# Kernel tuning notes

Measured on AMD Instinct MI355X. Metric: run time of the kernel, lower is better.

The kernel has to match this reference:

```python
import jax, jax.numpy as jnp
import numpy as np

N, K, A = 4096, 64, 8      # nodes, level-2 paths per node, attrs per l2-neighbor
D = 128                    # embed_dim
NU, NR, NA = 100000, 32, 5000  # user vocab, rating vocab, attribute vocab


def setup_inputs() -> dict:
    key = jax.random.key(0)
    ks = jax.random.split(key, 12)
    s = 0.02
    return dict(
        nodes=jax.random.randint(ks[0], (N,), 0, NU),
        paths_rel=jax.random.randint(ks[1], (N, K, 2), 0, NR),
        paths_nbr=jax.random.randint(ks[2], (N, K), 0, NU),
        attrs=jax.random.randint(ks[3], (N, K, A), 0, NA),
        u2e=jax.random.normal(ks[4], (NU, D), dtype=jnp.float32) * s,
        r2e=jax.random.normal(ks[5], (NR, D), dtype=jnp.float32) * s,
        ua2e=jax.random.normal(ks[6], (NA, D), dtype=jnp.float32) * s,
        W1=jax.random.normal(ks[7], (4 * D, 2 * D), dtype=jnp.float32) * s,
        b1=jnp.zeros((2 * D,), jnp.float32),
        W2=jax.random.normal(ks[8], (2 * D, D), dtype=jnp.float32) * s,
        b2=jnp.zeros((D,), jnp.float32),
        A1=jax.random.normal(ks[9], (2 * D, D), dtype=jnp.float32) * s,
        ab1=jnp.zeros((D,), jnp.float32),
        A2=jax.random.normal(ks[10], (D, D), dtype=jnp.float32) * s,
        ab2=jnp.zeros((D,), jnp.float32),
        A3=jax.random.normal(ks[11], (D, 1), dtype=jnp.float32) * s,
        ab3=jnp.zeros((1,), jnp.float32),
    )


def reference(nodes, paths_rel, paths_nbr, attrs, u2e, r2e, ua2e,
              W1, b1, W2, b2, A1, ab1, A2, ab2, A3, ab3):
    # per-path embedding gathers
    r1 = r2e[paths_rel[..., 0]]           # [N,K,D]
    r2 = r2e[paths_rel[..., 1]]           # [N,K,D]
    ne = u2e[paths_nbr]                   # [N,K,D]
    ae = ua2e[attrs].sum(axis=2)          # [N,K,A,D] -> [N,K,D] (uvAttrEmbedding sum)
    # concat + 2-layer MLP (w_r1, w_r2)
    x = jnp.concatenate([r1, r2, ne, ae], axis=-1)   # [N,K,4D]
    h = jax.nn.relu(x @ W1 + b1)                     # [N,K,2D]
    h = jax.nn.relu(h @ W2 + b2)                     # [N,K,D]
    # attention vs self embedding
    self_e = u2e[nodes]                              # [N,D]
    c = jnp.concatenate(
        [h, jnp.broadcast_to(self_e[:, None, :], h.shape)], axis=-1)  # [N,K,2D]
    a = jax.nn.relu(c @ A1 + ab1)
    a = jax.nn.relu(a @ A2 + ab2)
    logits = (a @ A3 + ab3)[..., 0]                  # [N,K]
    w = jax.nn.softmax(logits, axis=1)
    # attention-weighted reduce over paths
    return jnp.einsum('nk,nkd->nd', w, h)            # [N,D]
```

## Files before the change

### kernel.cpp

```cpp
#include <hip/hip_runtime.h>
#include <hip/hip_bf16.h>

#define NN 4096
#define KK 64
#define AA 8
#define DD 128

#define XH_STRIDE 264
#define A_STRIDE  136
#define H2_STRIDE 136
#define XREG_SZ   16896

typedef __bf16 bf16x8 __attribute__((ext_vector_type(8)));
typedef __bf16 bf16x2 __attribute__((ext_vector_type(2)));
typedef float  f32x4  __attribute__((ext_vector_type(4)));

__device__ __forceinline__ short f2bf(float f) {
    unsigned u = __builtin_bit_cast(unsigned, f);
    u += 0x7FFFu + ((u >> 16) & 1u);
    return (short)(u >> 16);
}
__device__ __forceinline__ float bf2f(short s) {
    unsigned u = ((unsigned)(unsigned short)s) << 16;
    return __builtin_bit_cast(float, u);
}
__device__ __forceinline__ unsigned f2bf2(float a, float b) {
#if __has_builtin(__builtin_amdgcn_cvt_pk_bf16_f32)
    bf16x2 r = __builtin_amdgcn_cvt_pk_bf16_f32(a, b);
    return __builtin_bit_cast(unsigned, r);
#else
    return ((unsigned)(unsigned short)f2bf(a)) | (((unsigned)(unsigned short)f2bf(b)) << 16);
#endif
}
__device__ __forceinline__ void store_bf8(short* dst, float4 a, float4 b) {
    uint4 v;
    v.x = f2bf2(a.x, a.y); v.y = f2bf2(a.z, a.w);
    v.z = f2bf2(b.x, b.y); v.w = f2bf2(b.z, b.w);
    *(uint4*)dst = v;
}
__device__ __forceinline__ void store_bf4(short* dst, float4 a) {
    uint2 v;
    v.x = f2bf2(a.x, a.y); v.y = f2bf2(a.z, a.w);
    *(uint2*)dst = v;
}

__global__ void prep_all(const float* __restrict__ W1, const float* __restrict__ W2,
                         const float* __restrict__ A1, const float* __restrict__ A2,
                         const int* __restrict__ nodes, const float* __restrict__ u2e,
                         const float* __restrict__ ab1,
                         short* __restrict__ W1p, short* __restrict__ W2p,
                         short* __restrict__ A1p, short* __restrict__ A2p,
                         float* __restrict__ s1g)
{
    if (blockIdx.x < 768) {
        int t = blockIdx.x * 256 + threadIdx.x;
        const float* src; short* dst; int Ncols, ksl, idx;
        if (t < 131072)      { src = W1; dst = W1p; Ncols = 256; ksl = 4; idx = t; }
        else if (t < 163840) { src = W2; dst = W2p; Ncols = 128; ksl = 3; idx = t - 131072; }
        else if (t < 180224) { src = A1; dst = A1p; Ncols = 128; ksl = 2; idx = t - 163840; }
        else                 { src = A2; dst = A2p; Ncols = 128; ksl = 2; idx = t - 180224; }
        int j     = idx & 7;
        int lane  = (idx >> 3) & 63;
        int fi    = idx >> 9;
        int kstep = fi & ((1 << ksl) - 1);
        int ntile = fi >> ksl;
        int k  = kstep * 32 + (lane >> 4) * 8 + j;
        int nn = ntile * 16 + (lane & 15);
        dst[idx] = f2bf(src[(size_t)k * Ncols + nn]);
    } else {
        __shared__ float rows[8][DD];
        const int b = blockIdx.x - 768;
        {
            const int r  = threadIdx.x >> 5;
            const int c4 = (threadIdx.x & 31) * 4;
            const int node = nodes[b * 8 + r];
            *(float4*)&rows[r][c4] = *(const float4*)&u2e[(size_t)node * DD + c4];
        }
        __syncthreads();
        const int h = threadIdx.x >> 7;
        const int c = threadIdx.x & 127;
        const float ab = ab1[c];
        float acc[4] = {ab, ab, ab, ab};
        for (int i = 0; i < DD; ++i) {
            const float av = A1[(size_t)(DD + i) * DD + c];
#pragma unroll
            for (int j = 0; j < 4; ++j)
                acc[j] = fmaf(rows[h * 4 + j][i], av, acc[j]);
        }
#pragma unroll
        for (int j = 0; j < 4; ++j)
            s1g[(size_t)(b * 8 + h * 4 + j) * DD + c] = acc[j];
    }
}

__launch_bounds__(512, 4)
__global__ void l2agg_mfma(
    const int* __restrict__ paths_rel,
    const int* __restrict__ paths_nbr,
    const int* __restrict__ attrs,
    const float* __restrict__ u2e,
    const float* __restrict__ r2e,
    const float* __restrict__ ua2e,
    const float* __restrict__ b1,
    const float* __restrict__ b2,
    const float* __restrict__ ab2,
    const float* __restrict__ A3,
    const float* __restrict__ ab3,
    const short* __restrict__ W1p,
    const short* __restrict__ W2p,
    const short* __restrict__ A1p,
    const short* __restrict__ A2p,
    const float* __restrict__ s1g,
    float* __restrict__ out)
{
    __shared__ short xa[XREG_SZ];
    __shared__ short xb[XREG_SZ];
    __shared__ int idx_u[576];
    float* partials = (float*)idx_u;
    float* wts      = (float*)(idx_u + 512);

    const int n    = blockIdx.x;
    const int tid  = threadIdx.x;
    const int lane = tid & 63;
    const int wv   = tid >> 6;
    const int mr   = lane & 15;
    const int q    = lane >> 4;

    {
        const int* ab = attrs + (size_t)n * KK * AA;
        __builtin_amdgcn_global_load_lds(
            (const __attribute__((address_space(1))) void*)(ab + wv * 64 + lane),
            (__attribute__((address_space(3))) void*)(idx_u + wv * 64), 4, 0, 0);
        if (wv == 0) {
            const int* nb = paths_nbr + (size_t)n * KK;
            __builtin_amdgcn_global_load_lds(
                (const __attribute__((address_space(1))) void*)(nb + lane),
                (__attribute__((address_space(3))) void*)(idx_u + 512), 4, 0, 0);
        }
    }

#pragma unroll
    for (int pass = 0; pass < 2; ++pass) {
        const int p  = pass * 32 + (tid >> 4);
        const int t  = tid & 15;
        const int o  = t * 8;
        const int pk = n * KK + p;
        const int i0 = paths_rel[pk * 2 + 0];
        const int i1 = paths_rel[pk * 2 + 1];
        float4 r1a = *(const float4*)&r2e[(size_t)i0 * DD + o];
        float4 r1b = *(const float4*)&r2e[(size_t)i0 * DD + o + 4];
        float4 r2a = *(const float4*)&r2e[(size_t)i1 * DD + o];
        float4 r2b = *(const float4*)&r2e[(size_t)i1 * DD + o + 4];
        store_bf8(&xa[p * XH_STRIDE + o], r1a, r1b);
        store_bf8(&xa[p * XH_STRIDE + 128 + o], r2a, r2b);
    }
    __syncthreads();

    const short* W1b = W1p + wv * 2 * 16 * 512 + lane * 8;
    f32x4 acc1[4][2] = {};
    bf16x8 bfc[2], bfn[2];
#pragma unroll
    for (int nt = 0; nt < 2; ++nt) bfc[nt] = *(const bf16x8*)&W1b[nt * 8192];

    const int sp = tid >> 5;
    const int so = (tid & 31) * 4;

#pragma unroll
    for (int step = 0; step < 4; ++step) {
        const int p  = step * 16 + sp;
        const int nb = idx_u[512 + p];
        const int4 ai0 = *(const int4*)&idx_u[p * 8];
        const int4 ai1 = *(const int4*)&idx_u[p * 8 + 4];
        float4 nev = *(const float4*)&u2e[(size_t)nb * DD + so];
        float4 g0 = *(const float4*)&ua2e[(size_t)ai0.x * DD + so];
        float4 g1 = *(const float4*)&ua2e[(size_t)ai0.y * DD + so];
        float4 g2 = *(const float4*)&ua2e[(size_t)ai0.z * DD + so];
        float4 g3 = *(const float4*)&ua2e[(size_t)ai0.w * DD + so];
        {
            const int ks = 2 * step;
#pragma unroll
            for (int nt = 0; nt < 2; ++nt)
                bfn[nt] = *(const bf16x8*)&W1b[nt * 8192 + (ks + 1) * 512];
            bf16x8 af[4];
#pragma unroll
            for (int mt = 0; mt < 4; ++mt)
                af[mt] = *(const bf16x8*)&xa[(mt * 16 + mr) * XH_STRIDE + ks * 32 + q * 8];
#pragma unroll
            for (int nt = 0; nt < 2; ++nt)
#pragma unroll
                for (int mt = 0; mt < 4; ++mt)
                    acc1[mt][nt] = __builtin_amdgcn_mfma_f32_16x16x32_bf16(af[mt], bfc[nt], acc1[mt][nt], 0, 0, 0);
#pragma unroll
            for (int nt = 0; nt < 2; ++nt) bfc[nt] = bfn[nt];
        }
        float4 s4;
        s4.x = (g0.x + g1.x) + (g2.x + g3.x);
        s4.y = (g0.y + g1.y) + (g2.y + g3.y);
        s4.z = (g0.z + g1.z) + (g2.z + g3.z);
        s4.w = (g0.w + g1.w) + (g2.w + g3.w);
        store_bf4(&xb[p * XH_STRIDE + so], nev);
        float4 g4 = *(const float4*)&ua2e[(size_t)ai1.x * DD + so];
        float4 g5 = *(const float4*)&ua2e[(size_t)ai1.y * DD + so];
        float4 g6 = *(const float4*)&ua2e[(size_t)ai1.z * DD + so];
        float4 g7 = *(const float4*)&ua2e[(size_t)ai1.w * DD + so];
        {
            const int ks = 2 * step + 1;
#pragma unroll
            for (int nt = 0; nt < 2; ++nt)
                bfn[nt] = *(const bf16x8*)&W1b[nt * 8192 + (ks + 1) * 512];
            bf16x8 af[4];
#pragma unroll
            for (int mt = 0; mt < 4; ++mt)
                af[mt] = *(const bf16x8*)&xa[(mt * 16 + mr) * XH_STRIDE + ks * 32 + q * 8];
#pragma unroll
            for (int nt = 0; nt < 2; ++nt)
#pragma unroll
                for (int mt = 0; mt < 4; ++mt)
                    acc1[mt][nt] = __builtin_amdgcn_mfma_f32_16x16x32_bf16(af[mt], bfc[nt], acc1[mt][nt], 0, 0, 0);
#pragma unroll
            for (int nt = 0; nt < 2; ++nt) bfc[nt] = bfn[nt];
        }
        s4.x += (g4.x + g5.x) + (g6.x + g7.x);
        s4.y += (g4.y + g5.y) + (g6.y + g7.y);
        s4.z += (g4.z + g5.z) + (g6.z + g7.z);
        s4.w += (g4.w + g5.w) + (g6.w + g7.w);
        store_bf4(&xb[p * XH_STRIDE + 128 + so], s4);
    }
    __syncthreads();

#pragma unroll
    for (int ks = 8; ks < 16; ++ks) {
        if (ks < 15) {
#pragma unroll
            for (int nt = 0; nt < 2; ++nt)
                bfn[nt] = *(const bf16x8*)&W1b[nt * 8192 + (ks + 1) * 512];
        }
        bf16x8 af[4];
#pragma unroll
        for (int mt = 0; mt < 4; ++mt)
            af[mt] = *(const bf16x8*)&xb[(mt * 16 + mr) * XH_STRIDE + (ks - 8) * 32 + q * 8];
#pragma unroll
        for (int nt = 0; nt < 2; ++nt)
#pragma unroll
            for (int mt = 0; mt < 4; ++mt)
                acc1[mt][nt] = __builtin_amdgcn_mfma_f32_16x16x32_bf16(af[mt], bfc[nt], acc1[mt][nt], 0, 0, 0);
        if (ks < 15) {
#pragma unroll
            for (int nt = 0; nt < 2; ++nt) bfc[nt] = bfn[nt];
        }
    }

    const short* W2b = W2p + wv * 8 * 512 + lane * 8;
    bf16x8 g2c = *(const bf16x8*)&W2b[0], g2n;

#pragma unroll
    for (int nt = 0; nt < 2; ++nt) {
        const int col = (wv * 2 + nt) * 16 + mr;
        const float bb = b1[col];
#pragma unroll
        for (int mt = 0; mt < 4; ++mt)
#pragma unroll
            for (int r = 0; r < 4; r += 2) {
                unsigned pk2 = f2bf2(fmaxf(acc1[mt][nt][r] + bb, 0.f),
                                     fmaxf(acc1[mt][nt][r + 1] + bb, 0.f));
                xa[(mt * 16 + q * 4 + r)     * XH_STRIDE + col] = (short)pk2;
                xa[(mt * 16 + q * 4 + r + 1) * XH_STRIDE + col] = (short)(pk2 >> 16);
            }
    }
    __syncthreads();

    f32x4 acc2[4] = {};
#pragma unroll
    for (int ks = 0; ks < 8; ++ks) {
        if (ks < 7) g2n = *(const bf16x8*)&W2b[(ks + 1) * 512];
        bf16x8 af[4];
#pragma unroll
        for (int mt = 0; mt < 4; ++mt)
            af[mt] = *(const bf16x8*)&xa[(mt * 16 + mr) * XH_STRIDE + ks * 32 + q * 8];
#pragma unroll
        for (int mt = 0; mt < 4; ++mt)
            acc2[mt] = __builtin_amdgcn_mfma_f32_16x16x32_bf16(af[mt], g2c, acc2[mt], 0, 0, 0);
        if (ks < 7) g2c = g2n;
    }

    const short* A1b = A1p + wv * 4 * 512 + lane * 8;
    bf16x8 g3f[4];
#pragma unroll
    for (int ks = 0; ks < 4; ++ks) g3f[ks] = *(const bf16x8*)&A1b[ks * 512];
    const float s1v = s1g[(size_t)n * DD + wv * 16 + mr];

    {
        const int col = wv * 16 + mr;
        const float bb = b2[col];
#pragma unroll
        for (int mt = 0; mt < 4; ++mt)
#pragma unroll
            for (int r = 0; r < 4; r += 2) {
                unsigned pk2 = f2bf2(fmaxf(acc2[mt][r] + bb, 0.f),
                                     fmaxf(acc2[mt][r + 1] + bb, 0.f));
                xb[(mt * 16 + q * 4 + r)     * H2_STRIDE + col] = (short)pk2;
                xb[(mt * 16 + q * 4 + r + 1) * H2_STRIDE + col] = (short)(pk2 >> 16);
            }
    }
    __syncthreads();

    {
        f32x4 acc3[4];
#pragma unroll
        for (int mt = 0; mt < 4; ++mt) {
            acc3[mt][0] = s1v; acc3[mt][1] = s1v; acc3[mt][2] = s1v; acc3[mt][3] = s1v;
        }
#pragma unroll
        for (int ks = 0; ks < 4; ++ks) {
            bf16x8 af[4];
#pragma unroll
            for (int mt = 0; mt < 4; ++mt)
                af[mt] = *(const bf16x8*)&xb[(mt * 16 + mr) * H2_STRIDE + ks * 32 + q * 8];
#pragma unroll
            for (int mt = 0; mt < 4; ++mt)
                acc3[mt] = __builtin_amdgcn_mfma_f32_16x16x32_bf16(af[mt], g3f[ks], acc3[mt], 0, 0, 0);
        }
        const short* A2b = A2p + wv * 4 * 512 + lane * 8;
        bf16x8 g4f[4];
#pragma unroll
        for (int ks = 0; ks < 4; ++ks) g4f[ks] = *(const bf16x8*)&A2b[ks * 512];

        {
            const int col = wv * 16 + mr;
#pragma unroll
            for (int mt = 0; mt < 4; ++mt)
#pragma unroll
                for (int r = 0; r < 4; r += 2) {
                    unsigned pk2 = f2bf2(fmaxf(acc3[mt][r], 0.f),
                                         fmaxf(acc3[mt][r + 1], 0.f));
                    xa[(mt * 16 + q * 4 + r)     * A_STRIDE + col] = (short)pk2;
                    xa[(mt * 16 + q * 4 + r + 1) * A_STRIDE + col] = (short)(pk2 >> 16);
                }
        }
        __syncthreads();

        f32x4 acc4[4];
        {
            const float bv = ab2[wv * 16 + mr];
#pragma unroll
            for (int mt = 0; mt < 4; ++mt) {
                acc4[mt][0] = bv; acc4[mt][1] = bv; acc4[mt][2] = bv; acc4[mt][3] = bv;
            }
        }
#pragma unroll
        for (int ks = 0; ks < 4; ++ks) {
            bf16x8 af[4];
#pragma unroll
            for (int mt = 0; mt < 4; ++mt)
                af[mt] = *(const bf16x8*)&xa[(mt * 16 + mr) * A_STRIDE + ks * 32 + q * 8];
#pragma unroll
            for (int mt = 0; mt < 4; ++mt)
                acc4[mt] = __builtin_amdgcn_mfma_f32_16x16x32_bf16(af[mt], g4f[ks], acc4[mt], 0, 0, 0);
        }
        const float av = A3[wv * 16 + mr];
        float pl[4][4];
#pragma unroll
        for (int mt = 0; mt < 4; ++mt)
#pragma unroll
            for (int r = 0; r < 4; ++r)
                pl[mt][r] = fmaxf(acc4[mt][r], 0.f) * av;
#pragma unroll
        for (int off = 1; off < 16; off <<= 1)
#pragma unroll
            for (int mt = 0; mt < 4; ++mt)
#pragma unroll
                for (int r = 0; r < 4; ++r)
                    pl[mt][r] += __shfl_xor(pl[mt][r], off, 64);
        if (mr == 0) {
#pragma unroll
            for (int mt = 0; mt < 4; ++mt)
#pragma unroll
                for (int r = 0; r < 4; ++r)
                    partials[wv * KK + mt * 16 + q * 4 + r] = pl[mt][r];
        }
    }
    __syncthreads();

    if (tid < KK) {
        float l = ab3[0];
#pragma unroll
        for (int w = 0; w < 8; ++w) l += partials[w * KK + tid];
        float m = l;
#pragma unroll
        for (int off = 32; off > 0; off >>= 1) m = fmaxf(m, __shfl_xor(m, off, 64));
        float e = expf(l - m);
        float s = e;
#pragma unroll
        for (int off = 32; off > 0; off >>= 1) s += __shfl_xor(s, off, 64);
        wts[tid] = e / s;
    }
    __syncthreads();

    if (tid < DD) {
        float acc = 0.f;
#pragma unroll 8
        for (int k = 0; k < KK; ++k)
            acc = fmaf(wts[k], bf2f(xb[k * H2_STRIDE + tid]), acc);
        out[(size_t)n * DD + tid] = acc;
    }
}

extern "C" void kernel_launch(void* const* d_in, const int* in_sizes, int n_in,
                              void* d_out, int out_size, void* d_ws, size_t ws_size,
                              hipStream_t stream)
{
    const int*   nodes     = (const int*)d_in[0];
    const int*   paths_rel = (const int*)d_in[1];
    const int*   paths_nbr = (const int*)d_in[2];
    const int*   attrs     = (const int*)d_in[3];
    const float* u2e  = (const float*)d_in[4];
    const float* r2e  = (const float*)d_in[5];
    const float* ua2e = (const float*)d_in[6];
    const float* W1   = (const float*)d_in[7];
    const float* b1   = (const float*)d_in[8];
    const float* W2   = (const float*)d_in[9];
    const float* b2   = (const float*)d_in[10];
    const float* A1   = (const float*)d_in[11];
    const float* ab1  = (const float*)d_in[12];
    const float* A2   = (const float*)d_in[13];
    const float* ab2  = (const float*)d_in[14];
    const float* A3   = (const float*)d_in[15];
    const float* ab3  = (const float*)d_in[16];
    float* out = (float*)d_out;

    short* wsp = (short*)d_ws;
    short* W1p = wsp;
    short* W2p = wsp + 131072;
    short* A1p = wsp + 163840;
    short* A2p = wsp + 180224;
    float* s1g = (float*)((char*)d_ws + 393216);

    hipLaunchKernelGGL(prep_all, dim3(768 + 512), dim3(256), 0, stream,
                       W1, W2, A1, A2, nodes, u2e, ab1,
                       W1p, W2p, A1p, A2p, s1g);
    hipLaunchKernelGGL(l2agg_mfma, dim3(NN), dim3(512), 0, stream,
                       paths_rel, paths_nbr, attrs, u2e, r2e, ua2e,
                       b1, b2, ab2, A3, ab3,
                       W1p, W2p, A1p, A2p, s1g, out);
}
```

Before: 298.0 us.

## Reorder W1 first-half MFMA before gathers, retile W2 GEMM, parallelize final reduce

The first half of the W1 GEMM now runs as a tight MFMA loop, and the neighbor and attribute gathers happen afterwards, with each thread loading 8-wide vectors. This replaces the earlier interleaving of gathers with MFMA steps. The W2 GEMM is retiled so each wave computes a 2x2 block of 16x16 tiles instead of 4 M-tiles by 1 N-tile, which reuses A fragments across two B fragments. The softmax and weighted reduction now run redundantly in every wave: each wave recomputes the softmax over the 64 logits and reduces its own 16 columns with a shuffle reduction, which removes a barrier. The trade-off is that gather latency is no longer hidden behind matrix work, and the softmax is computed eight times.

```diff
diff --git a/kernel.cpp b/kernel.cpp
--- a/kernel.cpp
+++ b/kernel.cpp
@@ -37,11 +37,6 @@
     v.x = f2bf2(a.x, a.y); v.y = f2bf2(a.z, a.w);
     v.z = f2bf2(b.x, b.y); v.w = f2bf2(b.z, b.w);
     *(uint4*)dst = v;
-}
-__device__ __forceinline__ void store_bf4(short* dst, float4 a) {
-    uint2 v;
-    v.x = f2bf2(a.x, a.y); v.y = f2bf2(a.z, a.w);
-    *(uint2*)dst = v;
 }
 
 __global__ void prep_all(const float* __restrict__ W1, const float* __restrict__ W2,
@@ -115,9 +110,9 @@
 {
     __shared__ short xa[XREG_SZ];
     __shared__ short xb[XREG_SZ];
-    __shared__ int idx_u[576];
+    __shared__ int   idx_u[576];
+    __shared__ float wts8[512];
     float* partials = (float*)idx_u;
-    float* wts      = (float*)(idx_u + 512);
 
     const int n    = blockIdx.x;
     const int tid  = threadIdx.x;
@@ -161,79 +156,53 @@
     bf16x8 bfc[2], bfn[2];
 #pragma unroll
     for (int nt = 0; nt < 2; ++nt) bfc[nt] = *(const bf16x8*)&W1b[nt * 8192];
-
-    const int sp = tid >> 5;
-    const int so = (tid & 31) * 4;
-
-#pragma unroll
-    for (int step = 0; step < 4; ++step) {
-        const int p  = step * 16 + sp;
+#pragma unroll
+    for (int ks = 0; ks < 8; ++ks) {
+#pragma unroll
+        for (int nt = 0; nt < 2; ++nt)
+            bfn[nt] = *(const bf16x8*)&W1b[nt * 8192 + (ks + 1) * 512];
+        bf16x8 af[4];
+#pragma unroll
+        for (int mt = 0; mt < 4; ++mt)
+            af[mt] = *(const bf16x8*)&xa[(mt * 16 + mr) * XH_STRIDE + ks * 32 + q * 8];
+#pragma unroll
+        for (int nt = 0; nt < 2; ++nt)
+#pragma unroll
+            for (int mt = 0; mt < 4; ++mt)
+                acc1[mt][nt] = __builtin_amdgcn_mfma_f32_16x16x32_bf16(af[mt], bfc[nt], acc1[mt][nt], 0, 0, 0);
+#pragma unroll
+        for (int nt = 0; nt < 2; ++nt) bfc[nt] = bfn[nt];
+    }
+
+#pragma unroll
+    for (int pass = 0; pass < 2; ++pass) {
+        const int p  = pass * 32 + (tid >> 4);
+        const int t  = tid & 15;
+        const int o  = t * 8;
         const int nb = idx_u[512 + p];
-        const int4 ai0 = *(const int4*)&idx_u[p * 8];
-        const int4 ai1 = *(const int4*)&idx_u[p * 8 + 4];
-        float4 nev = *(const float4*)&u2e[(size_t)nb * DD + so];
-        float4 g0 = *(const float4*)&ua2e[(size_t)ai0.x * DD + so];
-        float4 g1 = *(const float4*)&ua2e[(size_t)ai0.y * DD + so];
-        float4 g2 = *(const float4*)&ua2e[(size_t)ai0.z * DD + so];
-        float4 g3 = *(const float4*)&ua2e[(size_t)ai0.w * DD + so];
-        {
-            const int ks = 2 * step;
+        float4 nea = *(const float4*)&u2e[(size_t)nb * DD + o];
+        float4 neb = *(const float4*)&u2e[(size_t)nb * DD + o + 4];
+        float4 aea = make_float4(0.f, 0.f, 0.f, 0.f);
+        float4 aeb = make_float4(0.f, 0.f, 0.f, 0.f);
+#pragma unroll
+        for (int a = 0; a < AA; ++a) {
+            const int ai = idx_u[p * AA + a];
+            float4 va = *(const float4*)&ua2e[(size_t)ai * DD + o];
+            float4 vb = *(const float4*)&ua2e[(size_t)ai * DD + o + 4];
+            aea.x += va.x; aea.y += va.y; aea.z += va.z; aea.w += va.w;
+            aeb.x += vb.x; aeb.y += vb.y; aeb.z += vb.z; aeb.w += vb.w;
+        }
+        store_bf8(&xb[p * XH_STRIDE + o], nea, neb);
+        store_bf8(&xb[p * XH_STRIDE + 128 + o], aea, aeb);
+    }
+    __syncthreads();
+
+#pragma unroll
+    for (int ks = 8; ks < 16; ++ks) {
+        if (ks < 15) {
 #pragma unroll
             for (int nt = 0; nt < 2; ++nt)
                 bfn[nt] = *(const bf16x8*)&W1b[nt * 8192 + (ks + 1) * 512];
-            bf16x8 af[4];
-#pragma unroll
-            for (int mt = 0; mt < 4; ++mt)
-                af[mt] = *(const bf16x8*)&xa[(mt * 16 + mr) * XH_STRIDE + ks * 32 + q * 8];
-#pragma unroll
-            for (int nt = 0; nt < 2; ++nt)
-#pragma unroll
-                for (int mt = 0; mt < 4; ++mt)
-                    acc1[mt][nt] = __builtin_amdgcn_mfma_f32_16x16x32_bf16(af[mt], bfc[nt], acc1[mt][nt], 0, 0, 0);
-#pragma unroll
-            for (int nt = 0; nt < 2; ++nt) bfc[nt] = bfn[nt];
-        }
-        float4 s4;
-        s4.x = (g0.x + g1.x) + (g2.x + g3.x);
-        s4.y = (g0.y + g1.y) + (g2.y + g3.y);
-        s4.z = (g0.z + g1.z) + (g2.z + g3.z);
-        s4.w = (g0.w + g1.w) + (g2.w + g3.w);
-        store_bf4(&xb[p * XH_STRIDE + so], nev);
-        float4 g4 = *(const float4*)&ua2e[(size_t)ai1.x * DD + so];
-        float4 g5 = *(const float4*)&ua2e[(size_t)ai1.y * DD + so];
-        float4 g6 = *(const float4*)&ua2e[(size_t)ai1.z * DD + so];
-        float4 g7 = *(const float4*)&ua2e[(size_t)ai1.w * DD + so];
-        {
-            const int ks = 2 * step + 1;
-#pragma unroll
-            for (int nt = 0; nt < 2; ++nt)
-                bfn[nt] = *(const bf16x8*)&W1b[nt * 8192 + (ks + 1) * 512];
-            bf16x8 af[4];
-#pragma unroll
-            for (int mt = 0; mt < 4; ++mt)
-                af[mt] = *(const bf16x8*)&xa[(mt * 16 + mr) * XH_STRIDE + ks * 32 + q * 8];
-#pragma unroll
-            for (int nt = 0; nt < 2; ++nt)
-#pragma unroll
-                for (int mt = 0; mt < 4; ++mt)
-                    acc1[mt][nt] = __builtin_amdgcn_mfma_f32_16x16x32_bf16(af[mt], bfc[nt], acc1[mt][nt], 0, 0, 0);
-#pragma unroll
-            for (int nt = 0; nt < 2; ++nt) bfc[nt] = bfn[nt];
-        }
-        s4.x += (g4.x + g5.x) + (g6.x + g7.x);
-        s4.y += (g4.y + g5.y) + (g6.y + g7.y);
-        s4.z += (g4.z + g5.z) + (g6.z + g7.z);
-        s4.w += (g4.w + g5.w) + (g6.w + g7.w);
-        store_bf4(&xb[p * XH_STRIDE + 128 + so], s4);
-    }
-    __syncthreads();
-
-#pragma unroll
-    for (int ks = 8; ks < 16; ++ks) {
-        if (ks < 15) {
-#pragma unroll
-            for (int nt = 0; nt < 2; ++nt)
-                bfn[nt] = *(const bf16x8*)&W1b[nt * 8192 + (ks + 1) * 512];
         }
         bf16x8 af[4];
 #pragma unroll
@@ -250,8 +219,12 @@
         }
     }
 
-    const short* W2b = W2p + wv * 8 * 512 + lane * 8;
-    bf16x8 g2c = *(const bf16x8*)&W2b[0], g2n;
+    const int mtb = (wv >> 2) * 2;
+    const int nt0 = (wv & 3) * 2;
+    const short* W2b = W2p + nt0 * 8 * 512 + lane * 8;
+    bf16x8 g2c[2], g2n[2];
+    g2c[0] = *(const bf16x8*)&W2b[0];
+    g2c[1] = *(const bf16x8*)&W2b[4096];
 
 #pragma unroll
     for (int nt = 0; nt < 2; ++nt) {
@@ -269,18 +242,23 @@
     }
     __syncthreads();
 
-    f32x4 acc2[4] = {};
+    f32x4 acc2[2][2] = {};
 #pragma unroll
     for (int ks = 0; ks < 8; ++ks) {
-        if (ks < 7) g2n = *(const bf16x8*)&W2b[(ks + 1) * 512];
-        bf16x8 af[4];
-#pragma unroll
-        for (int mt = 0; mt < 4; ++mt)
-            af[mt] = *(const bf16x8*)&xa[(mt * 16 + mr) * XH_STRIDE + ks * 32 + q * 8];
-#pragma unroll
-        for (int mt = 0; mt < 4; ++mt)
-            acc2[mt] = __builtin_amdgcn_mfma_f32_16x16x32_bf16(af[mt], g2c, acc2[mt], 0, 0, 0);
-        if (ks < 7) g2c = g2n;
+        if (ks < 7) {
+            g2n[0] = *(const bf16x8*)&W2b[(ks + 1) * 512];
+            g2n[1] = *(const bf16x8*)&W2b[4096 + (ks + 1) * 512];
+        }
+        bf16x8 af[2];
+#pragma unroll
+        for (int j = 0; j < 2; ++j)
+            af[j] = *(const bf16x8*)&xa[((mtb + j) * 16 + mr) * XH_STRIDE + ks * 32 + q * 8];
+#pragma unroll
+        for (int t2 = 0; t2 < 2; ++t2)
+#pragma unroll
+            for (int j = 0; j < 2; ++j)
+                acc2[j][t2] = __builtin_amdgcn_mfma_f32_16x16x32_bf16(af[j], g2c[t2], acc2[j][t2], 0, 0, 0);
+        if (ks < 7) { g2c[0] = g2n[0]; g2c[1] = g2n[1]; }
     }
 
     const short* A1b = A1p + wv * 4 * 512 + lane * 8;
@@ -289,17 +267,18 @@
     for (int ks = 0; ks < 4; ++ks) g3f[ks] = *(const bf16x8*)&A1b[ks * 512];
     const float s1v = s1g[(size_t)n * DD + wv * 16 + mr];
 
-    {
-        const int col = wv * 16 + mr;
+#pragma unroll
+    for (int t2 = 0; t2 < 2; ++t2) {
+        const int col = (nt0 + t2) * 16 + mr;
         const float bb = b2[col];
 #pragma unroll
-        for (int mt = 0; mt < 4; ++mt)
+        for (int j = 0; j < 2; ++j)
 #pragma unroll
             for (int r = 0; r < 4; r += 2) {
-                unsigned pk2 = f2bf2(fmaxf(acc2[mt][r] + bb, 0.f),
-                                     fmaxf(acc2[mt][r + 1] + bb, 0.f));
-                xb[(mt * 16 + q * 4 + r)     * H2_STRIDE + col] = (short)pk2;
-                xb[(mt * 16 + q * 4 + r + 1) * H2_STRIDE + col] = (short)(pk2 >> 16);
+                unsigned pk2 = f2bf2(fmaxf(acc2[j][t2][r] + bb, 0.f),
+                                     fmaxf(acc2[j][t2][r + 1] + bb, 0.f));
+                xb[((mtb + j) * 16 + q * 4 + r)     * H2_STRIDE + col] = (short)pk2;
+                xb[((mtb + j) * 16 + q * 4 + r + 1) * H2_STRIDE + col] = (short)(pk2 >> 16);
             }
     }
     __syncthreads();
@@ -381,10 +360,10 @@
     }
     __syncthreads();
 
-    if (tid < KK) {
+    {
         float l = ab3[0];
 #pragma unroll
-        for (int w = 0; w < 8; ++w) l += partials[w * KK + tid];
+        for (int w = 0; w < 8; ++w) l += partials[w * KK + lane];
         float m = l;
 #pragma unroll
         for (int off = 32; off > 0; off >>= 1) m = fmaxf(m, __shfl_xor(m, off, 64));
@@ -392,16 +371,17 @@
         float s = e;
 #pragma unroll
         for (int off = 32; off > 0; off >>= 1) s += __shfl_xor(s, off, 64);
-        wts[tid] = e / s;
-    }
-    __syncthreads();
-
-    if (tid < DD) {
+        wts8[wv * 64 + lane] = e / s;
+        const int col = wv * 16 + mr;
+        const float* wl = &wts8[wv * 64 + q * 16];
+        const short* hp = &xb[(q * 16) * H2_STRIDE + col];
         float acc = 0.f;
-#pragma unroll 8
-        for (int k = 0; k < KK; ++k)
-            acc = fmaf(wts[k], bf2f(xb[k * H2_STRIDE + tid]), acc);
-        out[(size_t)n * DD + tid] = acc;
+#pragma unroll
+        for (int j = 0; j < 16; ++j)
+            acc = fmaf(wl[j], bf2f(hp[j * H2_STRIDE]), acc);
+        acc += __shfl_xor(acc, 16, 64);
+        acc += __shfl_xor(acc, 32, 64);
+        if (q == 0) out[(size_t)n * DD + col] = acc;
     }
 }
 
```

Result: slower. 310.8 us (+4.3%).
